# Kernel tuning notes

Measured on AMD Instinct MI355X. Metric: run time of the kernel, lower is better.

## Reference

```python
import jax, jax.numpy as jnp
import numpy as np

D_MODEL = 1024
N_HEADS = 16
D_K = D_MODEL // N_HEADS
THETA = 10000.0
MAX_SEQ_LEN = 2048


def _rope_tables(seq_len):
    pos = jnp.arange(seq_len, dtype=jnp.float32)
    inv_freq = 1.0 / (THETA ** (jnp.arange(0, D_K, 2, dtype=jnp.float32) / D_K))
    ang = pos[:, None] * inv_freq[None, :]  # [T, D_K/2]
    return jnp.cos(ang), jnp.sin(ang)


def _apply_rope(x, cos, sin):
    # x: [..., T, D_K]; cos/sin: [T, D_K/2]
    x_even = x[..., ::2]
    x_odd = x[..., 1::2]
    r_even = x_even * cos - x_odd * sin
    r_odd = x_even * sin + x_odd * cos
    out = jnp.stack([r_even, r_odd], axis=-1)  # [..., T, D_K/2, 2]
    return out.reshape(x.shape)


def setup_inputs() -> dict:
    key = jax.random.key(0)
    ks = jax.random.split(key, 5)
    std = np.sqrt(2.0 / (D_MODEL + D_MODEL))
    x = jax.random.normal(ks[0], (2, 2048, D_MODEL), dtype=jnp.float32)
    w_q = jax.random.normal(ks[1], (D_MODEL, D_MODEL), dtype=jnp.float32) * std
    w_k = jax.random.normal(ks[2], (D_MODEL, D_MODEL), dtype=jnp.float32) * std
    w_v = jax.random.normal(ks[3], (D_MODEL, D_MODEL), dtype=jnp.float32) * std
    w_o = jax.random.normal(ks[4], (D_MODEL, D_MODEL), dtype=jnp.float32) * std
    return {"x": x, "w_q": w_q, "w_k": w_k, "w_v": w_v, "w_o": w_o}


def reference(x, w_q, w_k, w_v, w_o):
    B, T, _ = x.shape
    # projections: weight stored as [d_out, d_in], y = x @ W^T
    q = jnp.einsum('btd,od->bto', x, w_q)
    k = jnp.einsum('btd,od->bto', x, w_k)
    v = jnp.einsum('btd,od->bto', x, w_v)
    # split heads: [B, T, H*Dk] -> [B, H, T, Dk]
    q = q.reshape(B, T, N_HEADS, D_K).transpose(0, 2, 1, 3)
    k = k.reshape(B, T, N_HEADS, D_K).transpose(0, 2, 1, 3)
    v = v.reshape(B, T, N_HEADS, D_K).transpose(0, 2, 1, 3)
    cos, sin = _rope_tables(T)
    q = _apply_rope(q, cos, sin)
    k = _apply_rope(k, cos, sin)
    scores = jnp.einsum('bhqd,bhkd->bhqk', q, k) / np.sqrt(D_K).astype(np.float32)
    causal = jnp.tril(jnp.ones((T, T), dtype=bool))
    scores = jnp.where(causal, scores, -jnp.inf)
    attn = jax.nn.softmax(scores, axis=-1)
    out = jnp.einsum('bhqk,bhkd->bhqd', attn, v)
    out = out.transpose(0, 2, 1, 3).reshape(B, T, D_MODEL)
    return jnp.einsum('btd,od->bto', out, w_o)
```

## Files before the change

### kernel.cpp

```cpp
#include <hip/hip_runtime.h>
#include <hip/hip_bf16.h>

typedef __bf16 bf16_t;
typedef __bf16 bf16x8 __attribute__((ext_vector_type(8)));
typedef float f32x4 __attribute__((ext_vector_type(4)));
typedef short short4v __attribute__((ext_vector_type(4)));

#define D_MODEL 1024
#define T_SEQ 2048
#define NH 16
#define DKD 64
#define X_ELEMS (4194304u)
#define W_ELEMS (1048576u)
#define Q_SCALE 0.18033688011112042f

__device__ __forceinline__ void async16(const bf16_t* g, bf16_t* l) {
    __builtin_amdgcn_global_load_lds((const __attribute__((address_space(1))) void*)g,
                                     (__attribute__((address_space(3))) void*)l, 16, 0, 0);
}

__global__ __launch_bounds__(256) void convert_kernel(
    const float* __restrict__ x, const float* __restrict__ wq,
    const float* __restrict__ wk, const float* __restrict__ wv,
    const float* __restrict__ wo,
    bf16_t* __restrict__ xb, bf16_t* __restrict__ wqb, bf16_t* __restrict__ wkb,
    bf16_t* __restrict__ wvb, bf16_t* __restrict__ wob)
{
    size_t idx = ((size_t)blockIdx.x * 256 + threadIdx.x) * 4;
    const float* src; bf16_t* dst; size_t off;
    if (idx < X_ELEMS) { src = x; dst = xb; off = idx; }
    else {
        size_t r = idx - X_ELEMS;
        unsigned w = (unsigned)(r >> 20);
        off = r & (W_ELEMS - 1);
        src = (w == 0) ? wq : (w == 1) ? wk : (w == 2) ? wv : wo;
        dst = (w == 0) ? wqb : (w == 1) ? wkb : (w == 2) ? wvb : wob;
    }
    float4 v = *(const float4*)(src + off);
    union { bf16_t b[4]; short4v s; } u;
    u.b[0] = (bf16_t)v.x; u.b[1] = (bf16_t)v.y;
    u.b[2] = (bf16_t)v.z; u.b[3] = (bf16_t)v.w;
    *(short4v*)(dst + off) = u.s;
}

__global__ __launch_bounds__(256) void rope_kernel(float* __restrict__ cost, float* __restrict__ sint)
{
    int idx = blockIdx.x * 256 + threadIdx.x;
    int t = idx >> 5, i = idx & 31;
    float inv = expf(-0.28782313662425572f * (float)i);
    float ang = (float)t * inv;
    float s, c;
    sincosf(ang, &s, &c);
    cost[idx] = c; sint[idx] = s;
}

__global__ __launch_bounds__(256) void gemm_fused(
    const bf16_t* __restrict__ A,
    const bf16_t* __restrict__ W0, const bf16_t* __restrict__ W1, const bf16_t* __restrict__ W2,
    bf16_t* __restrict__ qout, bf16_t* __restrict__ kout, bf16_t* __restrict__ vout,
    const float* __restrict__ cost, const float* __restrict__ sint,
    float* __restrict__ fout, int modeBase)
{
    const int K = 1024;
    __shared__ bf16_t As[128 * 32];
    __shared__ bf16_t Bs[128 * 32];
    const int tid = threadIdx.x;
    const int wave = tid >> 6, lane = tid & 63;
    const int quad = lane >> 4, l16 = lane & 15;
    const int m0 = blockIdx.x * 128;
    const int n0 = blockIdx.y * 128;
    const int wm = (wave >> 1) * 64, wn = (wave & 1) * 64;
    const int mode = modeBase + blockIdx.z;
    const bf16_t* W = (mode == 1) ? W1 : (mode == 2) ? W2 : W0;

    const bf16_t* Afrag = (mode == 2) ? Bs : As;
    const bf16_t* Bfrag = (mode == 2) ? As : Bs;
    const int aoff = (mode == 2) ? wn : wm;
    const int boff = (mode == 2) ? wm : wn;

    const f32x4 fzero = {0.f, 0.f, 0.f, 0.f};
    f32x4 acc[4][4];
    #pragma unroll
    for (int i = 0; i < 4; ++i)
        #pragma unroll
        for (int j = 0; j < 4; ++j) acc[i][j] = fzero;

    for (int k0 = 0; k0 < K; k0 += 32) {
        __syncthreads();
        #pragma unroll
        for (int c = 0; c < 2; ++c) {
            int G = c * 256 + tid;
            int row = G >> 2, go = G & 3;
            async16(A + (size_t)(m0 + row) * K + (k0 + go * 8), As + (size_t)(c * 256 + wave * 64) * 8);
            async16(W + (size_t)(n0 + row) * K + (k0 + go * 8), Bs + (size_t)(c * 256 + wave * 64) * 8);
        }
        __syncthreads();
        bf16x8 af[4], bfv[4];
        #pragma unroll
        for (int mi = 0; mi < 4; ++mi)
            af[mi] = *(const bf16x8*)(Afrag + (aoff + mi * 16 + l16) * 32 + quad * 8);
        #pragma unroll
        for (int ni = 0; ni < 4; ++ni)
            bfv[ni] = *(const bf16x8*)(Bfrag + (boff + ni * 16 + l16) * 32 + quad * 8);
        #pragma unroll
        for (int mi = 0; mi < 4; ++mi)
            #pragma unroll
            for (int ni = 0; ni < 4; ++ni)
                acc[mi][ni] = __builtin_amdgcn_mfma_f32_16x16x32_bf16(af[mi], bfv[ni], acc[mi][ni], 0, 0, 0);
    }

    #pragma unroll
    for (int mi = 0; mi < 4; ++mi) {
        #pragma unroll
        for (int ni = 0; ni < 4; ++ni) {
            #pragma unroll
            for (int reg = 0; reg < 4; ++reg) {
                float v = acc[mi][ni][reg];
                if (mode == 2) {
                    int f   = n0 + wn + mi * 16 + quad * 4 + reg;
                    int tok = m0 + wm + ni * 16 + l16;
                    int t = tok & (T_SEQ - 1), b = tok >> 11;
                    int h = f >> 6, dk = f & 63;
                    vout[(((size_t)b * NH + h) * DKD + dk) * T_SEQ + t] = (bf16_t)v;
                } else {
                    int row = m0 + wm + mi * 16 + quad * 4 + reg;
                    int col = n0 + wn + ni * 16 + l16;
                    if (mode == 3) {
                        fout[(size_t)row * D_MODEL + col] = v;
                    } else {
                        int t = row & (T_SEQ - 1), b = row >> 11;
                        int h = col >> 6, dk = col & 63;
                        float vp = __shfl_xor(v, 1);
                        int fi = dk >> 1;
                        float c = cost[t * 32 + fi], s = sint[t * 32 + fi];
                        float r = (dk & 1) ? (vp * s + v * c) : (v * c - vp * s);
                        if (mode == 0) r *= Q_SCALE;
                        bf16_t* dst = (mode == 0) ? qout : kout;
                        dst[(((size_t)b * NH + h) * T_SEQ + t) * DKD + dk] = (bf16_t)r;
                    }
                }
            }
        }
    }
}

__global__ __launch_bounds__(64, 2) void attn_kernel(
    const bf16_t* __restrict__ Q, const bf16_t* __restrict__ Kb,
    const bf16_t* __restrict__ Vt, bf16_t* __restrict__ O)
{
    __shared__ bf16_t Pw[2][16 * 72];
    const int lane = threadIdx.x;
    const int quad = lane >> 4, l16 = lane & 15;
    const int bh = blockIdx.x;
    const int qw = (63 - (int)blockIdx.y) * 32;

    const bf16_t* kbase = Kb + (size_t)bh * T_SEQ * DKD;
    const bf16_t* vbase = Vt + (size_t)bh * DKD * T_SEQ;

    bf16x8 qf[2][2];
    #pragma unroll
    for (int j = 0; j < 2; ++j) {
        const bf16_t* qp = Q + ((size_t)bh * T_SEQ + qw + j * 16 + l16) * DKD;
        qf[j][0] = *(const bf16x8*)(qp + quad * 8);
        qf[j][1] = *(const bf16x8*)(qp + 32 + quad * 8);
    }
    const f32x4 fzero = {0.f, 0.f, 0.f, 0.f};
    f32x4 oacc[2][4];
    #pragma unroll
    for (int j = 0; j < 2; ++j)
        #pragma unroll
        for (int i = 0; i < 4; ++i) oacc[j][i] = fzero;
    float lsum[2] = {0.f, 0.f};

    const int nkt = (qw + 95) >> 6;

    bf16x8 kcur[4][2], knxt[4][2], vcur[4][2];
    #pragma unroll
    for (int fi = 0; fi < 4; ++fi) {
        const bf16_t* kr = kbase + (size_t)(fi * 16 + l16) * DKD + quad * 8;
        kcur[fi][0] = *(const bf16x8*)(kr);
        kcur[fi][1] = *(const bf16x8*)(kr + 32);
    }

    for (int kt = 0; kt < nkt; ++kt) {
        const int k0 = kt * 64;
        #pragma unroll
        for (int di = 0; di < 4; ++di) {
            const bf16_t* vr = vbase + (size_t)(di * 16 + l16) * T_SEQ + k0 + quad * 8;
            vcur[di][0] = *(const bf16x8*)(vr);
            vcur[di][1] = *(const bf16x8*)(vr + 32);
        }
        if (kt + 1 < nkt) {
            #pragma unroll
            for (int fi = 0; fi < 4; ++fi) {
                const bf16_t* kr = kbase + (size_t)(k0 + 64 + fi * 16 + l16) * DKD + quad * 8;
                knxt[fi][0] = *(const bf16x8*)(kr);
                knxt[fi][1] = *(const bf16x8*)(kr + 32);
            }
        }

        #pragma unroll
        for (int j = 0; j < 2; ++j) {
            if (k0 > qw + j * 16 + 15) continue;
            const int qcol = qw + j * 16 + l16;
            f32x4 s[4];
            #pragma unroll
            for (int fi = 0; fi < 4; ++fi) {
                f32x4 z = fzero;
                z = __builtin_amdgcn_mfma_f32_16x16x32_bf16(kcur[fi][0], qf[j][0], z, 0, 0, 0);
                z = __builtin_amdgcn_mfma_f32_16x16x32_bf16(kcur[fi][1], qf[j][1], z, 0, 0, 0);
                s[fi] = z;
            }
            if (k0 + 63 > qw + j * 16) {
                #pragma unroll
                for (int fi = 0; fi < 4; ++fi)
                    #pragma unroll
                    for (int reg = 0; reg < 4; ++reg) {
                        int key = k0 + fi * 16 + quad * 4 + reg;
                        s[fi][reg] = (key > qcol) ? -__builtin_inff() : s[fi][reg];
                    }
            }
            float sm = 0.f;
            #pragma unroll
            for (int fi = 0; fi < 4; ++fi)
                #pragma unroll
                for (int reg = 0; reg < 4; ++reg) {
                    float p = __builtin_amdgcn_exp2f(s[fi][reg]);
                    s[fi][reg] = p;
                    sm += p;
                }
            lsum[j] += sm;

            bf16_t* pw = &Pw[j][0];
            #pragma unroll
            for (int fi = 0; fi < 4; ++fi) {
                union { bf16_t h[4]; unsigned long long u64; } pk;
                pk.h[0] = (bf16_t)s[fi][0]; pk.h[1] = (bf16_t)s[fi][1];
                pk.h[2] = (bf16_t)s[fi][2]; pk.h[3] = (bf16_t)s[fi][3];
                *(unsigned long long*)(pw + l16 * 72 + fi * 16 + quad * 4) = pk.u64;
            }
            bf16x8 pf[2];
            pf[0] = *(const bf16x8*)(pw + l16 * 72 + quad * 8);
            pf[1] = *(const bf16x8*)(pw + l16 * 72 + 32 + quad * 8);

            #pragma unroll
            for (int di = 0; di < 4; ++di) {
                oacc[j][di] = __builtin_amdgcn_mfma_f32_16x16x32_bf16(vcur[di][0], pf[0], oacc[j][di], 0, 0, 0);
                oacc[j][di] = __builtin_amdgcn_mfma_f32_16x16x32_bf16(vcur[di][1], pf[1], oacc[j][di], 0, 0, 0);
            }
        }

        if (kt + 1 < nkt) {
            #pragma unroll
            for (int fi = 0; fi < 4; ++fi) {
                kcur[fi][0] = knxt[fi][0];
                kcur[fi][1] = knxt[fi][1];
            }
        }
    }

    const int b = bh >> 4, h = bh & 15;
    #pragma unroll
    for (int j = 0; j < 2; ++j) {
        float l = lsum[j];
        l += __shfl_xor(l, 16);
        l += __shfl_xor(l, 32);
        float rl = 1.0f / l;
        int q = qw + j * 16 + l16;
        #pragma unroll
        for (int di = 0; di < 4; ++di) {
            union { bf16_t hh[4]; unsigned long long u64; } ok;
            #pragma unroll
            for (int reg = 0; reg < 4; ++reg) ok.hh[reg] = (bf16_t)(oacc[j][di][reg] * rl);
            int d = di * 16 + quad * 4;
            *(unsigned long long*)(O + ((size_t)b * T_SEQ + q) * D_MODEL + h * DKD + d) = ok.u64;
        }
    }
}

extern "C" void kernel_launch(void* const* d_in, const int* in_sizes, int n_in,
                              void* d_out, int out_size, void* d_ws, size_t ws_size,
                              hipStream_t stream)
{
    const float* x  = (const float*)d_in[0];
    const float* wq = (const float*)d_in[1];
    const float* wk = (const float*)d_in[2];
    const float* wv = (const float*)d_in[3];
    const float* wo = (const float*)d_in[4];
    float* out = (float*)d_out;

    char* ws = (char*)d_ws;
    size_t off = 0;
    auto alloc = [&](size_t bytes) -> void* {
        void* p = ws + off; off += (bytes + 255) & ~(size_t)255; return p;
    };
    bf16_t* xb   = (bf16_t*)alloc((size_t)X_ELEMS * 2);
    bf16_t* wqb  = (bf16_t*)alloc((size_t)W_ELEMS * 2);
    bf16_t* wkb  = (bf16_t*)alloc((size_t)W_ELEMS * 2);
    bf16_t* wvb  = (bf16_t*)alloc((size_t)W_ELEMS * 2);
    bf16_t* wob  = (bf16_t*)alloc((size_t)W_ELEMS * 2);
    bf16_t* qb   = (bf16_t*)alloc((size_t)X_ELEMS * 2);
    bf16_t* kb   = (bf16_t*)alloc((size_t)X_ELEMS * 2);
    bf16_t* vtb  = (bf16_t*)alloc((size_t)X_ELEMS * 2);
    bf16_t* ob   = (bf16_t*)alloc((size_t)X_ELEMS * 2);
    float*  cost = (float*)alloc((size_t)T_SEQ * 32 * 4);
    float*  sint = (float*)alloc((size_t)T_SEQ * 32 * 4);

    convert_kernel<<<8192, 256, 0, stream>>>(x, wq, wk, wv, wo, xb, wqb, wkb, wvb, wob);
    rope_kernel<<<256, 256, 0, stream>>>(cost, sint);
    gemm_fused<<<dim3(32, 8, 3), 256, 0, stream>>>(xb, wqb, wkb, wvb, qb, kb, vtb, cost, sint, nullptr, 0);
    attn_kernel<<<dim3(32, 64), 64, 0, stream>>>(qb, kb, vtb, ob);
    gemm_fused<<<dim3(32, 8, 1), 256, 0, stream>>>(ob, wob, nullptr, nullptr, nullptr, nullptr, nullptr,
                                                   cost, sint, out, 3);
}
```

Baseline: 219.5 us.

## Split attention KV tiles across four waves and split-K the output projection

The attention kernel now runs 256 threads per block. Each of the four waves handles every fourth 64-key tile, and waves 1-3 pass their partial output accumulators and row sums through shared memory so wave 0 can combine them. Separately, the output-projection GEMM is split over K into two halves. The second half writes a partial result into the reused Q buffer, and a new add kernel sums it into the output. This is meant to raise parallelism and occupancy for the latency-bound attention and the small 256-block final GEMM, at the cost of a shared-memory reduction, an extra kernel launch, and extra fp32 traffic for the partial sums.

```diff
diff --git a/kernel.cpp b/kernel.cpp
--- a/kernel.cpp
+++ b/kernel.cpp
@@ -59,9 +59,8 @@
     const bf16_t* __restrict__ W0, const bf16_t* __restrict__ W1, const bf16_t* __restrict__ W2,
     bf16_t* __restrict__ qout, bf16_t* __restrict__ kout, bf16_t* __restrict__ vout,
     const float* __restrict__ cost, const float* __restrict__ sint,
-    float* __restrict__ fout, int modeBase)
-{
-    const int K = 1024;
+    float* __restrict__ fout, float* __restrict__ fpart, int modeBase)
+{
     __shared__ bf16_t As[128 * 32];
     __shared__ bf16_t Bs[128 * 32];
     const int tid = threadIdx.x;
@@ -70,7 +69,10 @@
     const int m0 = blockIdx.x * 128;
     const int n0 = blockIdx.y * 128;
     const int wm = (wave >> 1) * 64, wn = (wave & 1) * 64;
-    const int mode = modeBase + blockIdx.z;
+    const int mode = (modeBase == 3) ? 3 : (modeBase + blockIdx.z);
+    const int kz = (modeBase == 3) ? blockIdx.z : 0;
+    const int kBeg = kz * 512;
+    const int kEnd = (modeBase == 3) ? (kBeg + 512) : 1024;
     const bf16_t* W = (mode == 1) ? W1 : (mode == 2) ? W2 : W0;
 
     const bf16_t* Afrag = (mode == 2) ? Bs : As;
@@ -85,14 +87,14 @@
         #pragma unroll
         for (int j = 0; j < 4; ++j) acc[i][j] = fzero;
 
-    for (int k0 = 0; k0 < K; k0 += 32) {
+    for (int k0 = kBeg; k0 < kEnd; k0 += 32) {
         __syncthreads();
         #pragma unroll
         for (int c = 0; c < 2; ++c) {
             int G = c * 256 + tid;
             int row = G >> 2, go = G & 3;
-            async16(A + (size_t)(m0 + row) * K + (k0 + go * 8), As + (size_t)(c * 256 + wave * 64) * 8);
-            async16(W + (size_t)(n0 + row) * K + (k0 + go * 8), Bs + (size_t)(c * 256 + wave * 64) * 8);
+            async16(A + (size_t)(m0 + row) * 1024 + (k0 + go * 8), As + (size_t)(c * 256 + wave * 64) * 8);
+            async16(W + (size_t)(n0 + row) * 1024 + (k0 + go * 8), Bs + (size_t)(c * 256 + wave * 64) * 8);
         }
         __syncthreads();
         bf16x8 af[4], bfv[4];
@@ -126,7 +128,8 @@
                     int row = m0 + wm + mi * 16 + quad * 4 + reg;
                     int col = n0 + wn + ni * 16 + l16;
                     if (mode == 3) {
-                        fout[(size_t)row * D_MODEL + col] = v;
+                        float* fo = kz ? fpart : fout;
+                        fo[(size_t)row * D_MODEL + col] = v;
                     } else {
                         int t = row & (T_SEQ - 1), b = row >> 11;
                         int h = col >> 6, dk = col & 63;
@@ -144,15 +147,28 @@
     }
 }
 
-__global__ __launch_bounds__(64, 2) void attn_kernel(
+__global__ __launch_bounds__(256) void add_kernel(float* __restrict__ out, const float* __restrict__ part)
+{
+    size_t i = ((size_t)blockIdx.x * 256 + threadIdx.x) * 4;
+    float4 o = *(const float4*)(out + i);
+    float4 p = *(const float4*)(part + i);
+    o.x += p.x; o.y += p.y; o.z += p.z; o.w += p.w;
+    *(float4*)(out + i) = o;
+}
+
+__global__ __launch_bounds__(256, 2) void attn_kernel(
     const bf16_t* __restrict__ Q, const bf16_t* __restrict__ Kb,
     const bf16_t* __restrict__ Vt, bf16_t* __restrict__ O)
 {
-    __shared__ bf16_t Pw[2][16 * 72];
-    const int lane = threadIdx.x;
+    __shared__ float Ocomb[3][2][4][4][16][4];
+    __shared__ float Lcomb[3][2][64];
+    __shared__ bf16_t Pw[4][16 * 72];
+    const int tid = threadIdx.x;
+    const int wave = tid >> 6, lane = tid & 63;
     const int quad = lane >> 4, l16 = lane & 15;
     const int bh = blockIdx.x;
-    const int qw = (63 - (int)blockIdx.y) * 32;
+    const int qb = 63 - (int)blockIdx.y;
+    const int qw = qb * 32;
 
     const bf16_t* kbase = Kb + (size_t)bh * T_SEQ * DKD;
     const bf16_t* vbase = Vt + (size_t)bh * DKD * T_SEQ;
@@ -177,12 +193,12 @@
     bf16x8 kcur[4][2], knxt[4][2], vcur[4][2];
     #pragma unroll
     for (int fi = 0; fi < 4; ++fi) {
-        const bf16_t* kr = kbase + (size_t)(fi * 16 + l16) * DKD + quad * 8;
+        const bf16_t* kr = kbase + (size_t)(wave * 64 + fi * 16 + l16) * DKD + quad * 8;
         kcur[fi][0] = *(const bf16x8*)(kr);
         kcur[fi][1] = *(const bf16x8*)(kr + 32);
     }
 
-    for (int kt = 0; kt < nkt; ++kt) {
+    for (int kt = wave; kt < nkt; kt += 4) {
         const int k0 = kt * 64;
         #pragma unroll
         for (int di = 0; di < 4; ++di) {
@@ -190,10 +206,10 @@
             vcur[di][0] = *(const bf16x8*)(vr);
             vcur[di][1] = *(const bf16x8*)(vr + 32);
         }
-        if (kt + 1 < nkt) {
+        if (kt + 4 < nkt) {
             #pragma unroll
             for (int fi = 0; fi < 4; ++fi) {
-                const bf16_t* kr = kbase + (size_t)(k0 + 64 + fi * 16 + l16) * DKD + quad * 8;
+                const bf16_t* kr = kbase + (size_t)((kt + 4) * 64 + fi * 16 + l16) * DKD + quad * 8;
                 knxt[fi][0] = *(const bf16x8*)(kr);
                 knxt[fi][1] = *(const bf16x8*)(kr + 32);
             }
@@ -231,7 +247,7 @@
                 }
             lsum[j] += sm;
 
-            bf16_t* pw = &Pw[j][0];
+            bf16_t* pw = &Pw[wave][0];
             #pragma unroll
             for (int fi = 0; fi < 4; ++fi) {
                 union { bf16_t h[4]; unsigned long long u64; } pk;
@@ -250,12 +266,38 @@
             }
         }
 
-        if (kt + 1 < nkt) {
+        if (kt + 4 < nkt) {
             #pragma unroll
             for (int fi = 0; fi < 4; ++fi) {
                 kcur[fi][0] = knxt[fi][0];
                 kcur[fi][1] = knxt[fi][1];
             }
+        }
+    }
+
+    if (wave > 0) {
+        #pragma unroll
+        for (int j = 0; j < 2; ++j) {
+            #pragma unroll
+            for (int di = 0; di < 4; ++di)
+                *(f32x4*)&Ocomb[wave - 1][j][di][quad][l16][0] = oacc[j][di];
+            Lcomb[wave - 1][j][lane] = lsum[j];
+        }
+    }
+    __syncthreads();
+    if (wave != 0) return;
+
+    #pragma unroll
+    for (int j = 0; j < 2; ++j) {
+        #pragma unroll
+        for (int w = 0; w < 3; ++w) {
+            #pragma unroll
+            for (int di = 0; di < 4; ++di) {
+                f32x4 p = *(const f32x4*)&Ocomb[w][j][di][quad][l16][0];
+                #pragma unroll
+                for (int reg = 0; reg < 4; ++reg) oacc[j][di][reg] += p[reg];
+            }
+            lsum[j] += Lcomb[w][j][lane];
         }
     }
 
@@ -305,11 +347,14 @@
     bf16_t* ob   = (bf16_t*)alloc((size_t)X_ELEMS * 2);
     float*  cost = (float*)alloc((size_t)T_SEQ * 32 * 4);
     float*  sint = (float*)alloc((size_t)T_SEQ * 32 * 4);
+    float*  fpart = (float*)qb;
 
     convert_kernel<<<8192, 256, 0, stream>>>(x, wq, wk, wv, wo, xb, wqb, wkb, wvb, wob);
     rope_kernel<<<256, 256, 0, stream>>>(cost, sint);
-    gemm_fused<<<dim3(32, 8, 3), 256, 0, stream>>>(xb, wqb, wkb, wvb, qb, kb, vtb, cost, sint, nullptr, 0);
-    attn_kernel<<<dim3(32, 64), 64, 0, stream>>>(qb, kb, vtb, ob);
-    gemm_fused<<<dim3(32, 8, 1), 256, 0, stream>>>(ob, wob, nullptr, nullptr, nullptr, nullptr, nullptr,
-                                                   cost, sint, out, 3);
-}
+    gemm_fused<<<dim3(32, 8, 3), 256, 0, stream>>>(xb, wqb, wkb, wvb, qb, kb, vtb, cost, sint,
+                                                   nullptr, nullptr, 0);
+    attn_kernel<<<dim3(32, 64), 256, 0, stream>>>(qb, kb, vtb, ob);
+    gemm_fused<<<dim3(32, 8, 2), 256, 0, stream>>>(ob, wob, nullptr, nullptr, nullptr, nullptr, nullptr,
+                                                   cost, sint, out, fpart, 3);
+    add_kernel<<<4096, 256, 0, stream>>>(out, fpart);
+}
```

Result: slower. 227.7 us (+3.7%).
